# Kernel tuning notes

Measured on AMD Instinct MI355X. Metric: run time of the kernel, lower is better.

## Reference

```python
import jax, jax.numpy as jnp
import numpy as np

N_NODES = 100000
N_EDGES = 1600000
IN_DIM = 128
HIDDEN = 128
EPS = 1e-5  # BatchNorm1d default eps


def gcn_conv(x, src, dst, W, b, n_nodes):
    """PyG GCNConv with default add_self_loops=True, edge_weight=None.
    out = D^{-1/2} (A + I) D^{-1/2} X W + b, deg computed from dst (col)."""
    xw = x @ W  # [N, out_dim] -- transform before propagate, as in PyG
    ones = jnp.ones((src.shape[0],), dtype=x.dtype)
    deg = jax.ops.segment_sum(ones, dst, num_segments=n_nodes) + 1.0  # +1 self-loop
    dis = jax.lax.rsqrt(deg)  # deg >= 1 always
    norm = dis[src] * dis[dst]  # [E]
    msgs = xw[src] * norm[:, None]  # [E, out_dim] gather (irregular access)
    agg = jax.ops.segment_sum(msgs, dst, num_segments=n_nodes)
    agg = agg + xw * (1.0 / deg)[:, None]  # self-loop contribution, norm = 1/deg_i
    return agg + b


def batch_norm(x, gamma, beta):
    # training-mode BatchNorm1d: biased batch statistics over the node dim
    m = jnp.mean(x, axis=0)
    v = jnp.mean(jnp.square(x - m), axis=0)
    return gamma * (x - m) * jax.lax.rsqrt(v + EPS) + beta


def setup_inputs() -> dict:
    key = jax.random.key(0)
    ks = jax.random.split(key, 6)
    x = jax.random.normal(ks[0], (N_NODES, IN_DIM), dtype=jnp.float32)
    edge_index = jax.random.randint(ks[1], (2, N_EDGES), 0, N_NODES, dtype=jnp.int64)
    # Glorot-ish scaled weights
    W1 = jax.random.normal(ks[2], (IN_DIM, HIDDEN), dtype=jnp.float32) / np.sqrt(IN_DIM)
    W2 = jax.random.normal(ks[3], (HIDDEN, HIDDEN // 2), dtype=jnp.float32) / np.sqrt(HIDDEN)
    Wf = jax.random.normal(ks[4], (HIDDEN // 2, 1), dtype=jnp.float32) / np.sqrt(HIDDEN // 2)
    return {
        "x": x,
        "edge_index": edge_index,
        "W1": W1, "b1": jnp.zeros((HIDDEN,), jnp.float32),
        "g1": jnp.ones((HIDDEN,), jnp.float32), "beta1": jnp.zeros((HIDDEN,), jnp.float32),
        "W2": W2, "b2": jnp.zeros((HIDDEN // 2,), jnp.float32),
        "g2": jnp.ones((HIDDEN // 2,), jnp.float32), "beta2": jnp.zeros((HIDDEN // 2,), jnp.float32),
        "Wf": Wf, "bf": jnp.zeros((1,), jnp.float32),
    }


def reference(x, edge_index, W1, b1, g1, beta1, W2, b2, g2, beta2, Wf, bf):
    src, dst = edge_index[0], edge_index[1]
    n = x.shape[0]
    h = jax.nn.relu(batch_norm(gcn_conv(x, src, dst, W1, b1, n), g1, beta1))
    # dropout is identity in eval / correctness-baseline mode
    h = jax.nn.relu(batch_norm(gcn_conv(h, src, dst, W2, b2, n), g2, beta2))
    return h @ Wf + bf  # [N, 1]
```

## Files before the change

kernel.cpp:

```cpp
#include <hip/hip_runtime.h>

#define NN 100000
#define NE 1600000
#define D1 128
#define D2 64
#define BN_EPS 1e-5f
#define SCAN_CHUNK 512
#define NB_SCAN ((NN + SCAN_CHUNK - 1) / SCAN_CHUNK)

typedef unsigned int uint32;
typedef unsigned short ushort16;

__device__ __forceinline__ uint32 f2bf_pair(float a, float b) {
    uint32 ua = __float_as_uint(a), ub = __float_as_uint(b);
    ua = (ua + 0x7FFFu + ((ua >> 16) & 1u)) >> 16;
    ub = (ub + 0x7FFFu + ((ub >> 16) & 1u)) >> 16;
    return ua | (ub << 16);
}
__device__ __forceinline__ float bf_lo(uint32 v) { return __uint_as_float(v << 16); }
__device__ __forceinline__ float bf_hi(uint32 v) { return __uint_as_float(v & 0xFFFF0000u); }

__global__ __launch_bounds__(256) void cnt_k(const int* __restrict__ dst,
                                             int* __restrict__ cnt) {
    int i = blockIdx.x * 256 + threadIdx.x;
    if (i < NE) atomicAdd(&cnt[dst[i]], 1);
}

__global__ __launch_bounds__(256) void make_dis_k(const int* __restrict__ cnt,
                                                  float* __restrict__ dis) {
    int i = blockIdx.x * 256 + threadIdx.x;
    if (i < NN) dis[i] = rsqrtf((float)cnt[i] + 1.0f);
}

__global__ __launch_bounds__(SCAN_CHUNK) void scan1_k(const int* __restrict__ cnt,
                                                      int* __restrict__ rowptr,
                                                      int* __restrict__ bsum) {
    __shared__ int sh[SCAN_CHUNK];
    int tid = threadIdx.x;
    int g = blockIdx.x * SCAN_CHUNK + tid;
    int v = (g < NN) ? cnt[g] : 0;
    sh[tid] = v;
    __syncthreads();
    for (int o = 1; o < SCAN_CHUNK; o <<= 1) {
        int t = (tid >= o) ? sh[tid - o] : 0;
        __syncthreads();
        sh[tid] += t;
        __syncthreads();
    }
    if (g < NN) rowptr[g] = sh[tid] - v;
    if (tid == SCAN_CHUNK - 1) bsum[blockIdx.x] = sh[tid];
}

__global__ void scan2_k(int* __restrict__ bsum) {
    if (threadIdx.x == 0 && blockIdx.x == 0) {
        int a = 0;
        for (int i = 0; i < NB_SCAN; ++i) { int t = bsum[i]; bsum[i] = a; a += t; }
    }
}

__global__ __launch_bounds__(256) void scan3_k(int* __restrict__ rowptr,
                                               const int* __restrict__ bsum) {
    int g = blockIdx.x * 256 + threadIdx.x;
    if (g < NN) rowptr[g] += bsum[g >> 9];
    if (g == 0) rowptr[NN] = NE;
}

__global__ __launch_bounds__(256) void fill_k(const int* __restrict__ src,
                                              const int* __restrict__ dst,
                                              const int* __restrict__ rowptr,
                                              const float* __restrict__ dis,
                                              int* __restrict__ cur,
                                              int* __restrict__ esrc,
                                              float* __restrict__ ew) {
    int e = blockIdx.x * 256 + threadIdx.x;
    if (e >= NE) return;
    int d = dst[e];
    int s = src[e];
    int p = rowptr[d] + atomicAdd(&cur[d], 1);
    esrc[p] = s;
    ew[p] = dis[s] * dis[d];
}

__global__ void bncoef_k(const float* __restrict__ sums, const float* __restrict__ ssq,
                         const float* __restrict__ g, const float* __restrict__ beta,
                         float* __restrict__ coef, int dim) {
    int c = threadIdx.x;
    if (c >= dim) return;
    float m = sums[c] * (1.0f / NN);
    float var = ssq[c] * (1.0f / NN) - m * m;
    float sc = g[c] * rsqrtf(var + BN_EPS);
    coef[c] = sc;
    coef[dim + c] = beta[c] - m * sc;
}

template<int OUT, bool FUSE_BN>
__global__ __launch_bounds__(256, 3) void gemm_k(const float* __restrict__ X,
                                                 const float* __restrict__ W,
                                                 const float* __restrict__ coef,
                                                 uint32* __restrict__ Yb) {
    constexpr int CG = OUT / 4;
    constexpr int RG = 256 / CG;
    constexpr int R  = 64 / RG;
    __shared__ float sW[32 * OUT];
    __shared__ float sc[128], sh[128];
    if constexpr (FUSE_BN) {
        if (threadIdx.x < 128) {
            sc[threadIdx.x] = coef[threadIdx.x];
            sh[threadIdx.x] = coef[128 + threadIdx.x];
        }
    }
    const int cg = threadIdx.x % CG;
    const int rg = threadIdx.x / CG;
    const int row0 = blockIdx.x * 64 + rg * R;
    int rows[R];
    #pragma unroll
    for (int r = 0; r < R; ++r) rows[r] = min(row0 + r, NN - 1);
    float acc[R][4];
    #pragma unroll
    for (int r = 0; r < R; ++r)
        acc[r][0] = acc[r][1] = acc[r][2] = acc[r][3] = 0.f;

    for (int kc = 0; kc < 128; kc += 32) {
        for (int i = threadIdx.x; i < 32 * OUT / 4; i += 256)
            ((float4*)sW)[i] = ((const float4*)(W + (size_t)kc * OUT))[i];
        __syncthreads();
        #pragma unroll 2
        for (int k = 0; k < 32; k += 4) {
            float4 xv[R];
            #pragma unroll
            for (int r = 0; r < R; ++r) {
                xv[r] = *(const float4*)(X + (size_t)rows[r] * 128 + kc + k);
                if constexpr (FUSE_BN) {
                    float4 s4 = *(const float4*)&sc[kc + k];
                    float4 h4 = *(const float4*)&sh[kc + k];
                    xv[r].x = fmaxf(fmaf(xv[r].x, s4.x, h4.x), 0.f);
                    xv[r].y = fmaxf(fmaf(xv[r].y, s4.y, h4.y), 0.f);
                    xv[r].z = fmaxf(fmaf(xv[r].z, s4.z, h4.z), 0.f);
                    xv[r].w = fmaxf(fmaf(xv[r].w, s4.w, h4.w), 0.f);
                }
            }
            #pragma unroll
            for (int kk = 0; kk < 4; ++kk) {
                float4 w = *(const float4*)&sW[(k + kk) * OUT + cg * 4];
                #pragma unroll
                for (int r = 0; r < R; ++r) {
                    float xs = ((const float*)&xv[r])[kk];
                    acc[r][0] = fmaf(xs, w.x, acc[r][0]);
                    acc[r][1] = fmaf(xs, w.y, acc[r][1]);
                    acc[r][2] = fmaf(xs, w.z, acc[r][2]);
                    acc[r][3] = fmaf(xs, w.w, acc[r][3]);
                }
            }
        }
        __syncthreads();
    }
    #pragma unroll
    for (int r = 0; r < R; ++r)
        if (row0 + r < NN) {
            uint32 p0 = f2bf_pair(acc[r][0], acc[r][1]);
            uint32 p1 = f2bf_pair(acc[r][2], acc[r][3]);
            *(uint2*)&Yb[(size_t)(row0 + r) * (OUT / 2) + cg * 2] = make_uint2(p0, p1);
        }
}

template<int DIM>
__global__ __launch_bounds__(256) void agg_k(const int* __restrict__ rowptr,
                                             const int* __restrict__ esrc,
                                             const float* __restrict__ ew,
                                             const float* __restrict__ dis,
                                             const uint32* __restrict__ xwb,
                                             const float* __restrict__ b,
                                             float* __restrict__ agg,
                                             float* __restrict__ sums,
                                             float* __restrict__ ssq) {
    const int lane = threadIdx.x & 63;
    const int wid = (blockIdx.x * 256 + threadIdx.x) >> 6;
    const int nwaves = gridDim.x * 4;
    float s0 = 0.f, s1 = 0.f, q0 = 0.f, q1 = 0.f;

    if constexpr (DIM == 128) {
        const float bc0 = b[lane * 2], bc1 = b[lane * 2 + 1];
        for (int n = wid; n < NN; n += nwaves) {
            const int beg = rowptr[n], end = rowptr[n + 1];
            const float dn = dis[n];
            float ax = 0.f, ay = 0.f;
            int e = beg;
            for (; e + 8 <= end; e += 8) {
                int idx[8]; float w[8]; uint32 vv[8];
                #pragma unroll
                for (int j = 0; j < 8; ++j) idx[j] = esrc[e + j];
                #pragma unroll
                for (int j = 0; j < 8; ++j) w[j] = ew[e + j];
                #pragma unroll
                for (int j = 0; j < 8; ++j)
                    vv[j] = xwb[(size_t)idx[j] * 64 + lane];
                #pragma unroll
                for (int j = 0; j < 8; ++j) {
                    ax = fmaf(bf_lo(vv[j]), w[j], ax);
                    ay = fmaf(bf_hi(vv[j]), w[j], ay);
                }
            }
            for (; e < end; ++e) {
                int s = esrc[e];
                float w = ew[e];
                uint32 v = xwb[(size_t)s * 64 + lane];
                ax = fmaf(bf_lo(v), w, ax);
                ay = fmaf(bf_hi(v), w, ay);
            }
            float sl = dn * dn;
            uint32 xv = xwb[(size_t)n * 64 + lane];
            ax = fmaf(bf_lo(xv), sl, ax) + bc0;
            ay = fmaf(bf_hi(xv), sl, ay) + bc1;
            *(float2*)&agg[(size_t)n * 128 + lane * 2] = make_float2(ax, ay);
            s0 += ax; q0 = fmaf(ax, ax, q0);
            s1 += ay; q1 = fmaf(ay, ay, q1);
        }
    } else {
        const ushort16* xws = (const ushort16*)xwb;
        const float bc0 = b[lane];
        for (int n = wid; n < NN; n += nwaves) {
            const int beg = rowptr[n], end = rowptr[n + 1];
            const float dn = dis[n];
            float ax = 0.f;
            int e = beg;
            for (; e + 8 <= end; e += 8) {
                int idx[8]; float w[8]; ushort16 vv[8];
                #pragma unroll
                for (int j = 0; j < 8; ++j) idx[j] = esrc[e + j];
                #pragma unroll
                for (int j = 0; j < 8; ++j) w[j] = ew[e + j];
                #pragma unroll
                for (int j = 0; j < 8; ++j)
                    vv[j] = xws[(size_t)idx[j] * 64 + lane];
                #pragma unroll
                for (int j = 0; j < 8; ++j)
                    ax = fmaf(__uint_as_float((uint32)vv[j] << 16), w[j], ax);
            }
            for (; e < end; ++e) {
                int s = esrc[e];
                ax = fmaf(__uint_as_float((uint32)xws[(size_t)s * 64 + lane] << 16),
                          ew[e], ax);
            }
            ax = fmaf(__uint_as_float((uint32)xws[(size_t)n * 64 + lane] << 16),
                      dn * dn, ax) + bc0;
            agg[(size_t)n * 64 + lane] = ax;
            s0 += ax; q0 = fmaf(ax, ax, q0);
        }
    }

    __shared__ float ls[2 * DIM];
    if (threadIdx.x < 2 * DIM) ls[threadIdx.x] = 0.f;
    __syncthreads();
    if constexpr (DIM == 128) {
        atomicAdd(&ls[lane * 2], s0);
        atomicAdd(&ls[lane * 2 + 1], s1);
        atomicAdd(&ls[DIM + lane * 2], q0);
        atomicAdd(&ls[DIM + lane * 2 + 1], q1);
    } else {
        atomicAdd(&ls[lane], s0);
        atomicAdd(&ls[DIM + lane], q0);
    }
    __syncthreads();
    if (threadIdx.x < DIM) atomicAdd(&sums[threadIdx.x], ls[threadIdx.x]);
    else if (threadIdx.x < 2 * DIM) atomicAdd(&ssq[threadIdx.x - DIM], ls[threadIdx.x]);
}

__global__ __launch_bounds__(256) void final_k(const float* __restrict__ h,
                                               const float* __restrict__ coef,
                                               const float* __restrict__ Wf,
                                               const float* __restrict__ bf,
                                               float* __restrict__ out) {
    int wid = (blockIdx.x * 256 + threadIdx.x) >> 6;
    int lane = threadIdx.x & 63;
    if (wid >= NN) return;
    float v = fmaxf(fmaf(h[(size_t)wid * 64 + lane], coef[lane], coef[64 + lane]), 0.f)
              * Wf[lane];
    #pragma unroll
    for (int o = 32; o > 0; o >>= 1) v += __shfl_down(v, o);
    if (lane == 0) out[wid] = v + bf[0];
}

extern "C" void kernel_launch(void* const* d_in, const int* in_sizes, int n_in,
                              void* d_out, int out_size, void* d_ws, size_t ws_size,
                              hipStream_t stream) {
    const float* x   = (const float*)d_in[0];
    const int*   ei  = (const int*)d_in[1];
    const int*   src = ei;
    const int*   dst = ei + NE;
    const float* W1  = (const float*)d_in[2];
    const float* b1  = (const float*)d_in[3];
    const float* g1  = (const float*)d_in[4];
    const float* be1 = (const float*)d_in[5];
    const float* W2  = (const float*)d_in[6];
    const float* b2  = (const float*)d_in[7];
    const float* g2  = (const float*)d_in[8];
    const float* be2 = (const float*)d_in[9];
    const float* Wf  = (const float*)d_in[10];
    const float* bf  = (const float*)d_in[11];
    float* out = (float*)d_out;

    uint32* xwb  = (uint32*)d_ws;
    float* agg1  = (float*)(xwb + (size_t)NN * 64);
    float* agg2  = agg1  + (size_t)NN * D1;
    float* dis   = agg2  + (size_t)NN * D2;
    float* sums1 = dis   + NN;
    float* ssq1  = sums1 + D1;
    float* sums2 = ssq1  + D1;
    float* ssq2  = sums2 + D2;
    float* coef1 = ssq2  + D2;
    float* coef2 = coef1 + 2 * D1;
    float* ew    = coef2 + 2 * D2;
    int*   cnt    = (int*)(ew + NE);
    int*   cur    = cnt + NN;
    int*   rowptr = cur + NN;
    int*   bsum   = rowptr + NN + 1;
    int*   esrc   = bsum + 256;

    hipMemsetAsync(cnt, 0, sizeof(int) * 2 * NN, stream);
    hipMemsetAsync(sums1, 0, sizeof(float) * (2 * D1 + 2 * D2), stream);

    cnt_k<<<(NE + 255) / 256, 256, 0, stream>>>(dst, cnt);
    make_dis_k<<<(NN + 255) / 256, 256, 0, stream>>>(cnt, dis);
    scan1_k<<<NB_SCAN, SCAN_CHUNK, 0, stream>>>(cnt, rowptr, bsum);
    scan2_k<<<1, 64, 0, stream>>>(bsum);
    scan3_k<<<(NN + 255) / 256, 256, 0, stream>>>(rowptr, bsum);
    fill_k<<<(NE + 255) / 256, 256, 0, stream>>>(src, dst, rowptr, dis, cur, esrc, ew);

    gemm_k<128, false><<<(NN + 63) / 64, 256, 0, stream>>>(x, W1, nullptr, xwb);
    agg_k<128><<<2048, 256, 0, stream>>>(rowptr, esrc, ew, dis, xwb, b1, agg1, sums1, ssq1);
    bncoef_k<<<1, 128, 0, stream>>>(sums1, ssq1, g1, be1, coef1, D1);

    gemm_k<64, true><<<(NN + 63) / 64, 256, 0, stream>>>(agg1, W2, coef1, xwb);
    agg_k<64><<<2048, 256, 0, stream>>>(rowptr, esrc, ew, dis, xwb, b2, agg2, sums2, ssq2);
    bncoef_k<<<1, 64, 0, stream>>>(sums2, ssq2, g2, be2, coef2, D2);

    final_k<<<(NN * 64 + 255) / 256, 256, 0, stream>>>(agg2, coef2, Wf, bf, out);
}
```

Before: 533.9 us.

## Pack CSR edges as 64-bit pairs, broadcast via shuffles, add nontemporal hints

Edge source index and normalisation weight are packed into one 64-bit word in the CSR fill. The aggregation loop loads 8 packed edges with one wave-wide load and broadcasts them with shuffles instead of issuing 16 separate uniform loads per chunk. Nontemporal loads and stores are added for streaming reads of GEMM input and the aggregation output, to keep the gathered features resident in cache. The shuffles add cross-lane traffic, and the nontemporal hints could hurt if agg is soon reread.

```diff
diff --git a/kernel.cpp b/kernel.cpp
--- a/kernel.cpp
+++ b/kernel.cpp
@@ -9,7 +9,8 @@
 #define NB_SCAN ((NN + SCAN_CHUNK - 1) / SCAN_CHUNK)
 
 typedef unsigned int uint32;
-typedef unsigned short ushort16;
+typedef unsigned long long u64;
+typedef float __attribute__((ext_vector_type(4))) f32x4;
 
 __device__ __forceinline__ uint32 f2bf_pair(float a, float b) {
     uint32 ua = __float_as_uint(a), ub = __float_as_uint(b);
@@ -19,6 +20,11 @@
 }
 __device__ __forceinline__ float bf_lo(uint32 v) { return __uint_as_float(v << 16); }
 __device__ __forceinline__ float bf_hi(uint32 v) { return __uint_as_float(v & 0xFFFF0000u); }
+
+__device__ __forceinline__ float4 nt_load4(const float* p) {
+    f32x4 v = __builtin_nontemporal_load((const f32x4*)p);
+    return make_float4(v.x, v.y, v.z, v.w);
+}
 
 __global__ __launch_bounds__(256) void cnt_k(const int* __restrict__ dst,
                                              int* __restrict__ cnt) {
@@ -70,15 +76,14 @@
                                               const int* __restrict__ rowptr,
                                               const float* __restrict__ dis,
                                               int* __restrict__ cur,
-                                              int* __restrict__ esrc,
-                                              float* __restrict__ ew) {
+                                              u64* __restrict__ edges) {
     int e = blockIdx.x * 256 + threadIdx.x;
     if (e >= NE) return;
     int d = dst[e];
     int s = src[e];
     int p = rowptr[d] + atomicAdd(&cur[d], 1);
-    esrc[p] = s;
-    ew[p] = dis[s] * dis[d];
+    u64 pk = ((u64)__float_as_uint(dis[s] * dis[d]) << 32) | (uint32)s;
+    edges[p] = pk;
 }
 
 __global__ void bncoef_k(const float* __restrict__ sums, const float* __restrict__ ssq,
@@ -129,7 +134,7 @@
             float4 xv[R];
             #pragma unroll
             for (int r = 0; r < R; ++r) {
-                xv[r] = *(const float4*)(X + (size_t)rows[r] * 128 + kc + k);
+                xv[r] = nt_load4(X + (size_t)rows[r] * 128 + kc + k);
                 if constexpr (FUSE_BN) {
                     float4 s4 = *(const float4*)&sc[kc + k];
                     float4 h4 = *(const float4*)&sh[kc + k];
@@ -165,8 +170,7 @@
 
 template<int DIM>
 __global__ __launch_bounds__(256) void agg_k(const int* __restrict__ rowptr,
-                                             const int* __restrict__ esrc,
-                                             const float* __restrict__ ew,
+                                             const u64* __restrict__ edges,
                                              const float* __restrict__ dis,
                                              const uint32* __restrict__ xwb,
                                              const float* __restrict__ b,
@@ -186,24 +190,24 @@
             float ax = 0.f, ay = 0.f;
             int e = beg;
             for (; e + 8 <= end; e += 8) {
-                int idx[8]; float w[8]; uint32 vv[8];
-                #pragma unroll
-                for (int j = 0; j < 8; ++j) idx[j] = esrc[e + j];
-                #pragma unroll
-                for (int j = 0; j < 8; ++j) w[j] = ew[e + j];
-                #pragma unroll
-                for (int j = 0; j < 8; ++j)
-                    vv[j] = xwb[(size_t)idx[j] * 64 + lane];
+                u64 ed = __builtin_nontemporal_load(&edges[e + (lane & 7)]);
+                uint32 vv[8]; float ww[8];
                 #pragma unroll
                 for (int j = 0; j < 8; ++j) {
-                    ax = fmaf(bf_lo(vv[j]), w[j], ax);
-                    ay = fmaf(bf_hi(vv[j]), w[j], ay);
+                    int s = __shfl((int)(uint32)ed, j);
+                    ww[j] = __uint_as_float((uint32)__shfl((int)(uint32)(ed >> 32), j));
+                    vv[j] = xwb[(size_t)s * 64 + lane];
+                }
+                #pragma unroll
+                for (int j = 0; j < 8; ++j) {
+                    ax = fmaf(bf_lo(vv[j]), ww[j], ax);
+                    ay = fmaf(bf_hi(vv[j]), ww[j], ay);
                 }
             }
             for (; e < end; ++e) {
-                int s = esrc[e];
-                float w = ew[e];
-                uint32 v = xwb[(size_t)s * 64 + lane];
+                u64 ed = edges[e];
+                float w = __uint_as_float((uint32)(ed >> 32));
+                uint32 v = xwb[(size_t)(uint32)ed * 64 + lane];
                 ax = fmaf(bf_lo(v), w, ax);
                 ay = fmaf(bf_hi(v), w, ay);
             }
@@ -211,12 +215,13 @@
             uint32 xv = xwb[(size_t)n * 64 + lane];
             ax = fmaf(bf_lo(xv), sl, ax) + bc0;
             ay = fmaf(bf_hi(xv), sl, ay) + bc1;
-            *(float2*)&agg[(size_t)n * 128 + lane * 2] = make_float2(ax, ay);
+            u64 o = ((u64)__float_as_uint(ay) << 32) | __float_as_uint(ax);
+            __builtin_nontemporal_store(o, (u64*)&agg[(size_t)n * 128 + lane * 2]);
             s0 += ax; q0 = fmaf(ax, ax, q0);
             s1 += ay; q1 = fmaf(ay, ay, q1);
         }
     } else {
-        const ushort16* xws = (const ushort16*)xwb;
+        const unsigned short* xws = (const unsigned short*)xwb;
         const float bc0 = b[lane];
         for (int n = wid; n < NN; n += nwaves) {
             const int beg = rowptr[n], end = rowptr[n + 1];
@@ -224,26 +229,27 @@
             float ax = 0.f;
             int e = beg;
             for (; e + 8 <= end; e += 8) {
-                int idx[8]; float w[8]; ushort16 vv[8];
-                #pragma unroll
-                for (int j = 0; j < 8; ++j) idx[j] = esrc[e + j];
-                #pragma unroll
-                for (int j = 0; j < 8; ++j) w[j] = ew[e + j];
+                u64 ed = __builtin_nontemporal_load(&edges[e + (lane & 7)]);
+                uint32 vv[8]; float ww[8];
+                #pragma unroll
+                for (int j = 0; j < 8; ++j) {
+                    int s = __shfl((int)(uint32)ed, j);
+                    ww[j] = __uint_as_float((uint32)__shfl((int)(uint32)(ed >> 32), j));
+                    vv[j] = (uint32)xws[(size_t)s * 64 + lane];
+                }
                 #pragma unroll
                 for (int j = 0; j < 8; ++j)
-                    vv[j] = xws[(size_t)idx[j] * 64 + lane];
-                #pragma unroll
-                for (int j = 0; j < 8; ++j)
-                    ax = fmaf(__uint_as_float((uint32)vv[j] << 16), w[j], ax);
+                    ax = fmaf(__uint_as_float(vv[j] << 16), ww[j], ax);
             }
             for (; e < end; ++e) {
-                int s = esrc[e];
-                ax = fmaf(__uint_as_float((uint32)xws[(size_t)s * 64 + lane] << 16),
-                          ew[e], ax);
+                u64 ed = edges[e];
+                float w = __uint_as_float((uint32)(ed >> 32));
+                ax = fmaf(__uint_as_float((uint32)xws[(size_t)(uint32)ed * 64 + lane] << 16),
+                          w, ax);
             }
             ax = fmaf(__uint_as_float((uint32)xws[(size_t)n * 64 + lane] << 16),
                       dn * dn, ax) + bc0;
-            agg[(size_t)n * 64 + lane] = ax;
+            __builtin_nontemporal_store(ax, &agg[(size_t)n * 64 + lane]);
             s0 += ax; q0 = fmaf(ax, ax, q0);
         }
     }
@@ -309,12 +315,11 @@
     float* ssq2  = sums2 + D2;
     float* coef1 = ssq2  + D2;
     float* coef2 = coef1 + 2 * D1;
-    float* ew    = coef2 + 2 * D2;
-    int*   cnt    = (int*)(ew + NE);
+    int*   cnt    = (int*)(coef2 + 2 * D2);
     int*   cur    = cnt + NN;
     int*   rowptr = cur + NN;
     int*   bsum   = rowptr + NN + 1;
-    int*   esrc   = bsum + 256;
+    u64*   edges  = (u64*)(((size_t)(bsum + 256) + 7) & ~(size_t)7);
 
     hipMemsetAsync(cnt, 0, sizeof(int) * 2 * NN, stream);
     hipMemsetAsync(sums1, 0, sizeof(float) * (2 * D1 + 2 * D2), stream);
@@ -324,14 +329,14 @@
     scan1_k<<<NB_SCAN, SCAN_CHUNK, 0, stream>>>(cnt, rowptr, bsum);
     scan2_k<<<1, 64, 0, stream>>>(bsum);
     scan3_k<<<(NN + 255) / 256, 256, 0, stream>>>(rowptr, bsum);
-    fill_k<<<(NE + 255) / 256, 256, 0, stream>>>(src, dst, rowptr, dis, cur, esrc, ew);
+    fill_k<<<(NE + 255) / 256, 256, 0, stream>>>(src, dst, rowptr, dis, cur, edges);
 
     gemm_k<128, false><<<(NN + 63) / 64, 256, 0, stream>>>(x, W1, nullptr, xwb);
-    agg_k<128><<<2048, 256, 0, stream>>>(rowptr, esrc, ew, dis, xwb, b1, agg1, sums1, ssq1);
+    agg_k<128><<<2048, 256, 0, stream>>>(rowptr, edges, dis, xwb, b1, agg1, sums1, ssq1);
     bncoef_k<<<1, 128, 0, stream>>>(sums1, ssq1, g1, be1, coef1, D1);
 
     gemm_k<64, true><<<(NN + 63) / 64, 256, 0, stream>>>(agg1, W2, coef1, xwb);
-    agg_k<64><<<2048, 256, 0, stream>>>(rowptr, esrc, ew, dis, xwb, b2, agg2, sums2, ssq2);
+    agg_k<64><<<2048, 256, 0, stream>>>(rowptr, edges, dis, xwb, b2, agg2, sums2, ssq2);
     bncoef_k<<<1, 64, 0, stream>>>(sums2, ssq2, g2, be2, coef2, D2);
 
     final_k<<<(NN * 64 + 255) / 256, 256, 0, stream>>>(agg2, coef2, Wf, bf, out);
```

Result: slower. 574.6 us (+7.6%).
